# Kernel optimization log

Hardware: AMD Instinct MI355X
Metric: run time of the kernel (lower is better)

Reference implementation:

```python
import jax, jax.numpy as jnp
import numpy as np

INPUT_SIZE = 32
HIDDEN = 512
LAYERS = 2
B, T = 16, 2048


def _lstm_layer(x, w_ih, w_hh, b_ih, b_hh):
    """Single LSTM layer, batch_first. x: [B,T,I]. Gate order (PyTorch): i,f,g,o."""
    Bsz = x.shape[0]
    H = w_hh.shape[1]
    # Precompute input contribution for all timesteps: [B,T,4H]
    gx = jnp.einsum('bti,gi->btg', x, w_ih) + b_ih

    def step(carry, gx_t):
        h, c = carry
        g = gx_t + h @ w_hh.T + b_hh  # [B,4H]
        i, f, gg, o = jnp.split(g, 4, axis=-1)
        i = jax.nn.sigmoid(i)
        f = jax.nn.sigmoid(f)
        gg = jnp.tanh(gg)
        o = jax.nn.sigmoid(o)
        c = f * c + i * gg
        h = o * jnp.tanh(c)
        return (h, c), h

    h0 = jnp.zeros((Bsz, H), x.dtype)
    (hT, cT), hs = jax.lax.scan(step, (h0, h0), jnp.swapaxes(gx, 0, 1))
    return jnp.swapaxes(hs, 0, 1), hT, cT  # [B,T,H], [B,H], [B,H]


def setup_inputs() -> dict:
    key = jax.random.key(0)
    ks = jax.random.split(key, 11)
    s = 1.0 / np.sqrt(HIDDEN)  # PyTorch uniform init scale
    u = lambda k, shape: jax.random.uniform(k, shape, jnp.float32, -s, s)
    return {
        'x': jax.random.normal(ks[0], (B, T, INPUT_SIZE), jnp.float32),
        'w_ih0': u(ks[1], (4 * HIDDEN, INPUT_SIZE)),
        'w_hh0': u(ks[2], (4 * HIDDEN, HIDDEN)),
        'b_ih0': u(ks[3], (4 * HIDDEN,)),
        'b_hh0': u(ks[4], (4 * HIDDEN,)),
        'w_ih1': u(ks[5], (4 * HIDDEN, HIDDEN)),
        'w_hh1': u(ks[6], (4 * HIDDEN, HIDDEN)),
        'b_ih1': u(ks[7], (4 * HIDDEN,)),
        'b_hh1': u(ks[8], (4 * HIDDEN,)),
        'w_out': u(ks[9], (INPUT_SIZE, HIDDEN)),
        'b_out': u(ks[10], (INPUT_SIZE,)),
    }


def reference(x, w_ih0, w_hh0, b_ih0, b_hh0, w_ih1, w_hh1, b_ih1, b_hh1, w_out, b_out):
    h1, hT0, cT0 = _lstm_layer(x, w_ih0, w_hh0, b_ih0, b_hh0)
    h2, hT1, cT1 = _lstm_layer(h1, w_ih1, w_hh1, b_ih1, b_hh1)
    y = jnp.einsum('bth,oh->bto', h2, w_out) + b_out  # [B,T,input_size]
    h_n = jnp.stack([hT0, hT1], axis=0)  # [layers, B, H]
    c_n = jnp.stack([cT0, cT1], axis=0)
    return y, h_n, c_n
```

## Files before the change

kernel.cpp:

```cpp
#include <hip/hip_runtime.h>

#define TT   2048
#define NB   16
#define HH   512
#define NSL  32
#define HSL  16
#define KW   128
#define Y_SZ (NB*TT*32)
#define RING 256
#define RM   255

typedef __attribute__((ext_vector_type(8))) short bf16x8;
typedef __attribute__((ext_vector_type(4))) float f32x4;
typedef __attribute__((ext_vector_type(4))) unsigned u32x4;
typedef unsigned long long ull;

#define OFF_XCCV 0u
#define OFF_MODE 256u
#define OFF_PROG 512u
#define OFF_F1L  4096u
#define FLB      (4u*RING*32u*4u)
#define OFF_F1X  (OFF_F1L + FLB)
#define OFF_F2L  (OFF_F1X + FLB)
#define OFF_F2X  (OFF_F2L + FLB)
#define OFF_ZEND (OFF_F2X + FLB)
#define RSLOT    ((size_t)NB*HH)
#define RB       ((size_t)RING*RSLOT*2)
#define OFF_H1LH ((size_t)(1u<<20))
#define OFF_H1LL (OFF_H1LH + RB)
#define OFF_H1XH (OFF_H1LL + RB)
#define OFF_H1XL (OFF_H1XH + RB)
#define OFF_H2LH (OFF_H1XL + RB)
#define OFF_H2LL (OFF_H2LH + RB)
#define OFF_H2XH (OFF_H2LL + RB)
#define OFF_H2XL (OFF_H2XH + RB)
#define FB       ((size_t)TT*RSLOT*2)
#define OFF_H2FH (OFF_H2XL + RB)
#define OFF_H2FL (OFF_H2FH + FB)
#define WS_NEED  (OFF_H2FL + FB)

__device__ __forceinline__ unsigned short f2bf(float x){
  unsigned u = __float_as_uint(x);
  return (unsigned short)((u + 0x7FFFu + ((u >> 16) & 1u)) >> 16);
}
__device__ __forceinline__ float bf2f(unsigned short b){
  return __uint_as_float(((unsigned)b) << 16);
}
__device__ __forceinline__ float sigm(float v){ return 1.0f / (1.0f + __expf(-v)); }
__device__ __forceinline__ float tanh_f(float v){
  float a = fabsf(v);
  float e = __expf(-2.0f * a);
  float t = (1.0f - e) / (1.0f + e);
  return v < 0.0f ? -t : t;
}
__device__ __forceinline__ void split8(const float* __restrict__ p, bf16x8& hi, bf16x8& lo){
#pragma unroll
  for (int j = 0; j < 8; ++j){
    float w = p[j];
    unsigned short h = f2bf(w);
    hi[j] = (short)h;
    lo[j] = (short)f2bf(w - bf2f(h));
  }
}
__device__ __forceinline__ bf16x8 mk(ull a, ull b){
  union { ull u[2]; bf16x8 v; } r; r.u[0] = a; r.u[1] = b; return r.v;
}
__device__ __forceinline__ bf16x8 asfrag(u32x4 v){
  union { u32x4 u; bf16x8 b; } r; r.u = v; return r.b;
}
__device__ __forceinline__ ull ld64_lic(const ull* p){
  return __hip_atomic_load(p, __ATOMIC_RELAXED, __HIP_MEMORY_SCOPE_AGENT);
}
__device__ __forceinline__ unsigned ld32_lic(const unsigned* p){
  return __hip_atomic_load(p, __ATOMIC_RELAXED, __HIP_MEMORY_SCOPE_AGENT);
}
__device__ __forceinline__ void st64_lic(ull* p, ull v){
  __hip_atomic_store(p, v, __ATOMIC_RELAXED, __HIP_MEMORY_SCOPE_AGENT);
}
__device__ __forceinline__ void st32_lic(unsigned* p, unsigned v){
  __hip_atomic_store(p, v, __ATOMIC_RELAXED, __HIP_MEMORY_SCOPE_AGENT);
}
__device__ __forceinline__ bf16x8 ld_frag_lic(const unsigned short* p){
  return mk(ld64_lic((const ull*)p), ld64_lic((const ull*)p + 1));
}
__device__ __forceinline__ unsigned ld32_l2(const unsigned* p){
  unsigned r;
  asm volatile("buffer_inv sc0\n\t"
               "global_load_dword %0, %1, off\n\t"
               "s_waitcnt vmcnt(0)"
               : "=&v"(r) : "v"(p) : "memory");
  return r;
}
__device__ __forceinline__ void ld8_l2(const void* ph, const void* pl, u32x4* r){
  asm volatile(
    "buffer_inv sc0\n\t"
    "global_load_dwordx4 %0, %8, off\n\t"
    "global_load_dwordx4 %1, %8, off offset:64\n\t"
    "global_load_dwordx4 %2, %8, off offset:128\n\t"
    "global_load_dwordx4 %3, %8, off offset:192\n\t"
    "global_load_dwordx4 %4, %9, off\n\t"
    "global_load_dwordx4 %5, %9, off offset:64\n\t"
    "global_load_dwordx4 %6, %9, off offset:128\n\t"
    "global_load_dwordx4 %7, %9, off offset:192\n\t"
    "s_waitcnt vmcnt(0)"
    : "=&v"(r[0]),"=&v"(r[1]),"=&v"(r[2]),"=&v"(r[3]),
      "=&v"(r[4]),"=&v"(r[5]),"=&v"(r[6]),"=&v"(r[7])
    : "v"(ph), "v"(pl) : "memory");
}
__device__ __forceinline__ void ld8_lic(const void* ph, const void* pl, u32x4* r){
  asm volatile(
    "global_load_dwordx4 %0, %8, off sc0 sc1\n\t"
    "global_load_dwordx4 %1, %8, off offset:64 sc0 sc1\n\t"
    "global_load_dwordx4 %2, %8, off offset:128 sc0 sc1\n\t"
    "global_load_dwordx4 %3, %8, off offset:192 sc0 sc1\n\t"
    "global_load_dwordx4 %4, %9, off sc0 sc1\n\t"
    "global_load_dwordx4 %5, %9, off offset:64 sc0 sc1\n\t"
    "global_load_dwordx4 %6, %9, off offset:128 sc0 sc1\n\t"
    "global_load_dwordx4 %7, %9, off offset:192 sc0 sc1\n\t"
    "s_waitcnt vmcnt(0)"
    : "=&v"(r[0]),"=&v"(r[1]),"=&v"(r[2]),"=&v"(r[3]),
      "=&v"(r[4]),"=&v"(r[5]),"=&v"(r[6]),"=&v"(r[7])
    : "v"(ph), "v"(pl) : "memory");
}
__device__ __forceinline__ void st64_pl(void* p, ull v){
  asm volatile("global_store_dwordx2 %0, %1, off" :: "v"(p), "v"(v) : "memory");
}
__device__ __forceinline__ void st32_pl(unsigned* p, unsigned v){
  asm volatile("global_store_dword %0, %1, off" :: "v"(p), "v"(v) : "memory");
}

__device__ __forceinline__ int wait_hy(const unsigned* bL, const unsigned* bX,
                                       unsigned expect, int lane, int lmode, long& bud){
  if (!lmode){
    bool ok = (lane >= 32);
    while (__ballot(!ok) != 0ULL){
      if (!ok) ok = (ld32_lic(bX + lane) >= expect);
      if (--bud < 0) return 0;
    }
    return 0;
  }
  bool okL = (lane >= 32);
  int k = 0;
  while (true){
    if (__ballot(!okL) == 0ULL) return 1;
    if (!okL) okL = (ld32_l2(bL + lane) >= expect);
    if ((++k & 15) == 0){
      bool okX = (lane >= 32);
      if (!okX) okX = (ld32_lic(bX + lane) >= expect);
      if (__ballot(!okX) == 0ULL){
        if (!okL) okL = (ld32_l2(bL + lane) >= expect);
        return (__ballot(!okL) == 0ULL) ? 1 : 0;
      }
    }
    if (--bud < 0) return 0;
  }
}
__device__ __forceinline__ void wait_lic(const unsigned* bX, unsigned expect, int lane, long& bud){
  bool ok = (lane >= 32);
  while (__ballot(!ok) != 0ULL){
    if (!ok) ok = (ld32_lic(bX + lane) >= expect);
    if (--bud < 0) return;
  }
}

__global__ __launch_bounds__(256, 1) void lstm_persist(
    const float* __restrict__ x,
    const float* __restrict__ w_ih0, const float* __restrict__ w_hh0,
    const float* __restrict__ b_ih0, const float* __restrict__ b_hh0,
    const float* __restrict__ w_ih1, const float* __restrict__ w_hh1,
    const float* __restrict__ b_ih1, const float* __restrict__ b_hh1,
    float* __restrict__ out, unsigned char* __restrict__ ws)
{
  unsigned* XCCV = (unsigned*)(ws + OFF_XCCV);
  unsigned* MODE = (unsigned*)(ws + OFF_MODE);
  unsigned* PROG = (unsigned*)(ws + OFF_PROG);
  unsigned* F1L  = (unsigned*)(ws + OFF_F1L);
  unsigned* F1X  = (unsigned*)(ws + OFF_F1X);
  unsigned* F2L  = (unsigned*)(ws + OFF_F2L);
  unsigned* F2X  = (unsigned*)(ws + OFF_F2X);
  unsigned short* H1Lh = (unsigned short*)(ws + OFF_H1LH);
  unsigned short* H1Ll = (unsigned short*)(ws + OFF_H1LL);
  unsigned short* H1Xh = (unsigned short*)(ws + OFF_H1XH);
  unsigned short* H1Xl = (unsigned short*)(ws + OFF_H1XL);
  unsigned short* H2Lh = (unsigned short*)(ws + OFF_H2LH);
  unsigned short* H2Ll = (unsigned short*)(ws + OFF_H2LL);
  unsigned short* H2Xh = (unsigned short*)(ws + OFF_H2XH);
  unsigned short* H2Xl = (unsigned short*)(ws + OFF_H2XL);
  unsigned short* H2Fh = (unsigned short*)(ws + OFF_H2FH);
  unsigned short* H2Fl = (unsigned short*)(ws + OFF_H2FL);

  const int tid  = threadIdx.x;
  const int lane = tid & 63;
  const int wv   = tid >> 6;
  const int m16  = lane & 15;
  const int quad = lane >> 4;

  const int bid = blockIdx.x;
  const int xs  = bid & 7;
  const int pos = bid >> 3;
  if (xs >= 2 || pos >= NSL) return;
  const int layer = xs;
  const int sl    = pos;
  const int role  = layer * NSL + sl;
  const int j0    = sl * HSL;
  const int kwb   = wv * KW;

  long bud = 3000000;

  if (tid == 0){
    unsigned xcc = 0xDEAD;
    asm volatile("s_getreg_b32 %0, hwreg(HW_REG_XCC_ID)" : "=s"(xcc));
    st32_lic(XCCV + role, (xcc & 255u) | 0x100u);
  }
  __syncthreads();
  if (bid == 0 && wv == 0){
    bool got = false; unsigned v = 0;
    long b2 = 2000000;
    while (true){
      if (!got){ v = ld32_lic(XCCV + lane); got = (v & 0x100u) != 0u; }
      if (__ballot(!got) == 0ULL) break;
      if (--b2 < 0) break;
    }
    unsigned v0  = (unsigned)__shfl((int)v, 0, 64);
    unsigned v32 = (unsigned)__shfl((int)v, 32, 64);
    bool ok = got && ((lane < 32) ? (v == v0) : (v == v32));
    unsigned mode = (__ballot(!ok) == 0ULL) ? 1u : 0u;
    if (lane == 0) st32_lic(MODE, mode | 0x100u);
  }
  __shared__ unsigned s_mode;
  if (tid == 0){
    unsigned m = 0; long b3 = 2000000;
    do { m = ld32_lic(MODE); } while (!(m & 0x100u) && --b3 > 0);
    s_mode = m;
  }
  __syncthreads();
  int lmode = ((s_mode & 0x100u) && (s_mode & 1u)) ? 1 : 0;

  const float* Wh  = layer ? w_hh1 : w_hh0;
  const float* biL = layer ? b_ih1 : b_ih0;
  const float* bhL = layer ? b_hh1 : b_hh0;

  bf16x8 Bh_hi[4][4], Bh_lo[4][4];
#pragma unroll
  for (int g = 0; g < 4; ++g)
#pragma unroll
    for (int c = 0; c < 4; ++c){
      int row = g*HH + j0 + m16;
      int k0  = kwb + c*32 + quad*8;
      split8(Wh + (size_t)row*HH + k0, Bh_hi[g][c], Bh_lo[g][c]);
    }
  bf16x8 Bi_hi[4][4], Bi_lo[4][4];
  if (layer){
#pragma unroll
    for (int g = 0; g < 4; ++g)
#pragma unroll
      for (int c = 0; c < 4; ++c){
        int row = g*HH + j0 + m16;
        int k0  = kwb + c*32 + quad*8;
        split8(w_ih1 + (size_t)row*HH + k0, Bi_hi[g][c], Bi_lo[g][c]);
      }
  } else if (wv == 0){
#pragma unroll
    for (int g = 0; g < 4; ++g){
      int row = g*HH + j0 + m16;
      split8(w_ih0 + (size_t)row*32 + quad*8, Bi_hi[g][0], Bi_lo[g][0]);
    }
  }

  const int eb = tid >> 4;
  const int ej = tid & 15;
  float bias[4];
#pragma unroll
  for (int g = 0; g < 4; ++g){
    int r = g*HH + j0 + ej;
    bias[g] = biL[r] + bhL[r];
  }

  float cst = 0.0f;
  __shared__ float P[4][4][16][16];
  unsigned minp = 0;

  f32x4 accIn[4];
#pragma unroll
  for (int g = 0; g < 4; ++g) accIn[g] = f32x4{0.f, 0.f, 0.f, 0.f};
  if (layer){
    wait_lic(F1X + ((size_t)wv*RING + 1)*32, 1u, lane, bud);
    const size_t ib = ((size_t)1*NB + m16)*HH + kwb + quad*8;
    u32x4 r[8];
    ld8_lic(H1Xh + ib, H1Xl + ib, r);
#pragma unroll
    for (int c = 0; c < 4; ++c){
      bf16x8 ah = asfrag(r[c]);
      bf16x8 al = asfrag(r[4+c]);
#pragma unroll
      for (int g = 0; g < 4; ++g){
        accIn[g] = __builtin_amdgcn_mfma_f32_16x16x32_bf16(ah, Bi_hi[g][c], accIn[g], 0, 0, 0);
        accIn[g] = __builtin_amdgcn_mfma_f32_16x16x32_bf16(al, Bi_hi[g][c], accIn[g], 0, 0, 0);
        accIn[g] = __builtin_amdgcn_mfma_f32_16x16x32_bf16(ah, Bi_lo[g][c], accIn[g], 0, 0, 0);
      }
    }
  }

  for (int t = 0; t < TT; ++t){
    const unsigned srec = (unsigned)t & RM;
    const unsigned spub = (unsigned)(t+1) & RM;
    f32x4 acc[4];

    if (layer == 0){
#pragma unroll
      for (int g = 0; g < 4; ++g) acc[g] = f32x4{0.f, 0.f, 0.f, 0.f};
      if (wv == 0){
        const float* xp = x + ((size_t)m16*TT + t)*32 + quad*8;
        bf16x8 ah, al;
#pragma unroll
        for (int j = 0; j < 8; ++j){
          float v = xp[j];
          unsigned short h = f2bf(v);
          ah[j] = (short)h;
          al[j] = (short)f2bf(v - bf2f(h));
        }
#pragma unroll
        for (int g = 0; g < 4; ++g){
          acc[g] = __builtin_amdgcn_mfma_f32_16x16x32_bf16(ah, Bi_hi[g][0], acc[g], 0, 0, 0);
          acc[g] = __builtin_amdgcn_mfma_f32_16x16x32_bf16(al, Bi_hi[g][0], acc[g], 0, 0, 0);
          acc[g] = __builtin_amdgcn_mfma_f32_16x16x32_bf16(ah, Bi_lo[g][0], acc[g], 0, 0, 0);
        }
      }
      while ((long)(t+1) - (long)minp > 248L){
        unsigned v = (lane < 32) ? ld32_lic(PROG + lane) : 0xFFFFFFFFu;
        unsigned m = v;
#pragma unroll
        for (int o = 1; o < 32; o <<= 1){
          unsigned ov = (unsigned)__shfl_xor((int)m, o, 32);
          m = m < ov ? m : ov;
        }
        minp = (unsigned)__shfl((int)m, 0, 64);
        if (--bud < 0) break;
      }
      int got = lmode;
      if (t > 0){
        got = wait_hy(F1L + ((size_t)wv*RING + srec)*32,
                      F1X + ((size_t)wv*RING + srec)*32, (unsigned)t, lane, lmode, bud);
        if (!got) lmode = 0;
      }
      const size_t rb = ((size_t)srec*NB + m16)*HH + kwb + quad*8;
      u32x4 r[8];
      if (got) ld8_l2(H1Lh + rb, H1Ll + rb, r);
      else {
#pragma unroll
        for (int c = 0; c < 4; ++c){
          r[c]   = (u32x4)__builtin_bit_cast(u32x4, ld_frag_lic(H1Xh + rb + c*32));
          r[4+c] = (u32x4)__builtin_bit_cast(u32x4, ld_frag_lic(H1Xl + rb + c*32));
        }
      }
#pragma unroll
      for (int c = 0; c < 4; ++c){
        bf16x8 ah = asfrag(r[c]);
        bf16x8 al = asfrag(r[4+c]);
#pragma unroll
        for (int g = 0; g < 4; ++g){
          acc[g] = __builtin_amdgcn_mfma_f32_16x16x32_bf16(ah, Bh_hi[g][c], acc[g], 0, 0, 0);
          acc[g] = __builtin_amdgcn_mfma_f32_16x16x32_bf16(al, Bh_hi[g][c], acc[g], 0, 0, 0);
          acc[g] = __builtin_amdgcn_mfma_f32_16x16x32_bf16(ah, Bh_lo[g][c], acc[g], 0, 0, 0);
        }
      }
    } else {
#pragma unroll
      for (int g = 0; g < 4; ++g) acc[g] = accIn[g];
      int got = lmode;
      if (t > 0){
        got = wait_hy(F2L + ((size_t)wv*RING + srec)*32,
                      F2X + ((size_t)wv*RING + srec)*32, (unsigned)t, lane, lmode, bud);
        if (!got) lmode = 0;
      }
      const size_t rb = ((size_t)srec*NB + m16)*HH + kwb + quad*8;
      u32x4 r[8];
      if (got) ld8_l2(H2Lh + rb, H2Ll + rb, r);
      else {
#pragma unroll
        for (int c = 0; c < 4; ++c){
          r[c]   = (u32x4)__builtin_bit_cast(u32x4, ld_frag_lic(H2Xh + rb + c*32));
          r[4+c] = (u32x4)__builtin_bit_cast(u32x4, ld_frag_lic(H2Xl + rb + c*32));
        }
      }
#pragma unroll
      for (int c = 0; c < 4; ++c){
        bf16x8 ah = asfrag(r[c]);
        bf16x8 al = asfrag(r[4+c]);
#pragma unroll
        for (int g = 0; g < 4; ++g){
          acc[g] = __builtin_amdgcn_mfma_f32_16x16x32_bf16(ah, Bh_hi[g][c], acc[g], 0, 0, 0);
          acc[g] = __builtin_amdgcn_mfma_f32_16x16x32_bf16(al, Bh_hi[g][c], acc[g], 0, 0, 0);
          acc[g] = __builtin_amdgcn_mfma_f32_16x16x32_bf16(ah, Bh_lo[g][c], acc[g], 0, 0, 0);
        }
      }
    }

#pragma unroll
    for (int g = 0; g < 4; ++g)
#pragma unroll
      for (int r = 0; r < 4; ++r)
        P[wv][g][quad*4 + r][m16] = acc[g][r];
    __syncthreads();

    float G[4];
#pragma unroll
    for (int g = 0; g < 4; ++g)
      G[g] = P[0][g][eb][ej] + P[1][g][eb][ej] + P[2][g][eb][ej] + P[3][g][eb][ej] + bias[g];

    float gi = sigm(G[0]);
    float gf = sigm(G[1]);
    float gc = tanh_f(G[2]);
    float go = sigm(G[3]);
    cst = gf*cst + gi*gc;
    float h = go * tanh_f(cst);

    if (t == TT-1){
      size_t o = (size_t)layer*NB*HH + (size_t)eb*HH + (j0 + ej);
      out[Y_SZ + o] = h;
      out[Y_SZ + 2*NB*HH + o] = cst;
    }

    unsigned short hhi = f2bf(h);
    unsigned short hlo = f2bf(h - bf2f(hhi));
    ull h1s = (ull)(unsigned short)__shfl_down((int)hhi, 1, 64);
    ull h2s = (ull)(unsigned short)__shfl_down((int)hhi, 2, 64);
    ull h3s = (ull)(unsigned short)__shfl_down((int)hhi, 3, 64);
    ull l1s = (ull)(unsigned short)__shfl_down((int)hlo, 1, 64);
    ull l2s = (ull)(unsigned short)__shfl_down((int)hlo, 2, 64);
    ull l3s = (ull)(unsigned short)__shfl_down((int)hlo, 3, 64);
    if ((ej & 3) == 0){
      ull vh = (ull)hhi | (h1s << 16) | (h2s << 32) | (h3s << 48);
      ull vl = (ull)hlo | (l1s << 16) | (l2s << 32) | (l3s << 48);
      size_t pr = (((size_t)spub*NB + eb)*HH + (unsigned)(j0 + ej)) >> 2;
      if (layer == 0){
        st64_pl((ull*)H1Lh + pr, vh);
        st64_pl((ull*)H1Ll + pr, vl);
        st64_lic((ull*)H1Xh + pr, vh);
        st64_lic((ull*)H1Xl + pr, vl);
      } else {
        size_t pf_ = (((size_t)t*NB + eb)*HH + (unsigned)(j0 + ej)) >> 2;
        st64_pl((ull*)H2Lh + pr, vh);
        st64_pl((ull*)H2Ll + pr, vl);
        st64_pl((ull*)H2Fh + pf_, vh);
        st64_pl((ull*)H2Fl + pf_, vl);
        st64_lic((ull*)H2Xh + pr, vh);
        st64_lic((ull*)H2Xl + pr, vl);
      }
    }

    asm volatile("s_waitcnt vmcnt(2)" ::: "memory");
    __syncthreads();
    if (tid == 0){
      unsigned val = (unsigned)(t+1);
      unsigned* FL = layer ? F2L : F1L;
#pragma unroll
      for (int r2 = 0; r2 < 4; ++r2)
        st32_pl(FL + ((size_t)r2*RING + spub)*32 + sl, val);
    }
    asm volatile("s_waitcnt vmcnt(0)" ::: "memory");
    __syncthreads();
    if (tid == 0){
      unsigned val = (unsigned)(t+1);
      unsigned* FX = layer ? F2X : F1X;
#pragma unroll
      for (int r2 = 0; r2 < 4; ++r2)
        st32_lic(FX + ((size_t)r2*RING + spub)*32 + sl, val);
      if (layer) st32_lic(PROG + sl, val);
    }

    if (layer && t + 1 < TT){
#pragma unroll
      for (int g = 0; g < 4; ++g) accIn[g] = f32x4{0.f, 0.f, 0.f, 0.f};
      const unsigned nslot = (unsigned)(t+2) & RM;
      wait_lic(F1X + ((size_t)wv*RING + nslot)*32, (unsigned)(t+2), lane, bud);
      const size_t nb_ = ((size_t)nslot*NB + m16)*HH + kwb + quad*8;
      u32x4 r[8];
      ld8_lic(H1Xh + nb_, H1Xl + nb_, r);
#pragma unroll
      for (int c = 0; c < 4; ++c){
        bf16x8 ah = asfrag(r[c]);
        bf16x8 al = asfrag(r[4+c]);
#pragma unroll
        for (int g = 0; g < 4; ++g){
          accIn[g] = __builtin_amdgcn_mfma_f32_16x16x32_bf16(ah, Bi_hi[g][c], accIn[g], 0, 0, 0);
          accIn[g] = __builtin_amdgcn_mfma_f32_16x16x32_bf16(al, Bi_hi[g][c], accIn[g], 0, 0, 0);
          accIn[g] = __builtin_amdgcn_mfma_f32_16x16x32_bf16(ah, Bi_lo[g][c], accIn[g], 0, 0, 0);
        }
      }
    }
  }
}

__global__ __launch_bounds__(256, 1) void y_proj(
    const unsigned short* __restrict__ Hhi2, const unsigned short* __restrict__ Hlo2,
    const float* __restrict__ w_out, const float* __restrict__ b_out,
    float* __restrict__ out)
{
  __shared__ float hsh[NB][HH + 1];
  __shared__ float wsh[32][HH + 1];
  const int tid = threadIdx.x;
  const int t = blockIdx.x;

  for (int i = tid; i < 32*HH; i += 256){
    int o = i >> 9, k = i & (HH-1);
    wsh[o][k] = w_out[i];
  }
  for (int i = tid; i < NB*HH; i += 256){
    int b = i >> 9, k = i & (HH-1);
    size_t off = ((size_t)t*NB + b)*HH + k;
    hsh[b][k] = bf2f(Hhi2[off]) + bf2f(Hlo2[off]);
  }
  __syncthreads();

  const int o = tid & 31, bg = tid >> 5;
  float a0 = 0.f, a1 = 0.f;
  for (int k = 0; k < HH; ++k){
    float w = wsh[o][k];
    a0 += w * hsh[bg][k];
    a1 += w * hsh[bg + 8][k];
  }
  float bo = b_out[o];
  out[((size_t)bg*TT + t)*32 + o] = a0 + bo;
  out[((size_t)(bg+8)*TT + t)*32 + o] = a1 + bo;
}

extern "C" void kernel_launch(void* const* d_in, const int* in_sizes, int n_in,
                              void* d_out, int out_size, void* d_ws, size_t ws_size,
                              hipStream_t stream)
{
  (void)in_sizes; (void)n_in; (void)out_size;
  const float* x     = (const float*)d_in[0];
  const float* w_ih0 = (const float*)d_in[1];
  const float* w_hh0 = (const float*)d_in[2];
  const float* b_ih0 = (const float*)d_in[3];
  const float* b_hh0 = (const float*)d_in[4];
  const float* w_ih1 = (const float*)d_in[5];
  const float* w_hh1 = (const float*)d_in[6];
  const float* b_ih1 = (const float*)d_in[7];
  const float* b_hh1 = (const float*)d_in[8];
  const float* w_out = (const float*)d_in[9];
  const float* b_out = (const float*)d_in[10];
  float* out = (float*)d_out;
  unsigned char* ws = (unsigned char*)d_ws;

  if (ws_size < WS_NEED) return;

  hipMemsetAsync(ws, 0, OFF_ZEND, stream);
  hipMemsetAsync(ws + OFF_H1LH, 0, RSLOT*2, stream);
  hipMemsetAsync(ws + OFF_H1LL, 0, RSLOT*2, stream);
  hipMemsetAsync(ws + OFF_H1XH, 0, RSLOT*2, stream);
  hipMemsetAsync(ws + OFF_H1XL, 0, RSLOT*2, stream);
  hipMemsetAsync(ws + OFF_H2LH, 0, RSLOT*2, stream);
  hipMemsetAsync(ws + OFF_H2LL, 0, RSLOT*2, stream);
  hipMemsetAsync(ws + OFF_H2XH, 0, RSLOT*2, stream);
  hipMemsetAsync(ws + OFF_H2XL, 0, RSLOT*2, stream);

  lstm_persist<<<dim3(512), dim3(256), 0, stream>>>(
      x, w_ih0, w_hh0, b_ih0, b_hh0, w_ih1, w_hh1, b_ih1, b_hh1, out, ws);

  const unsigned short* H2Fh = (const unsigned short*)(ws + OFF_H2FH);
  const unsigned short* H2Fl = (const unsigned short*)(ws + OFF_H2FL);
  y_proj<<<dim3(TT), dim3(256), 0, stream>>>(H2Fh, H2Fl, w_out, b_out, out);
}
```

Measured before the change: 10.08 ms.

## Overlap layer-1 input prefetch with flag publish and batch cross-layer waits

For layer 1, the step now issues the next timestep's layer-0 hidden-state loads before the cross-block flag barrier, so they overlap with the F2X publish. It also waits for layer-0 progress up to 16 steps ahead, so the per-step flag polling happens only occasionally. The LDS scratch array is padded to 17 columns to avoid bank conflicts, and __syncthreads is replaced by raw s_barrier with explicit waitcnt. This adds ordering subtlety: the relaxed waitcnt counts and the raw barriers must still keep the memory visibility that the protocol needs.

```diff
diff --git a/kernel.cpp b/kernel.cpp
--- a/kernel.cpp
+++ b/kernel.cpp
@@ -118,6 +118,20 @@
     "global_load_dwordx4 %6, %9, off offset:128 sc0 sc1\n\t"
     "global_load_dwordx4 %7, %9, off offset:192 sc0 sc1\n\t"
     "s_waitcnt vmcnt(0)"
+    : "=&v"(r[0]),"=&v"(r[1]),"=&v"(r[2]),"=&v"(r[3]),
+      "=&v"(r[4]),"=&v"(r[5]),"=&v"(r[6]),"=&v"(r[7])
+    : "v"(ph), "v"(pl) : "memory");
+}
+__device__ __forceinline__ void ld8_lic_issue(const void* ph, const void* pl, u32x4* r){
+  asm volatile(
+    "global_load_dwordx4 %0, %8, off sc0 sc1\n\t"
+    "global_load_dwordx4 %1, %8, off offset:64 sc0 sc1\n\t"
+    "global_load_dwordx4 %2, %8, off offset:128 sc0 sc1\n\t"
+    "global_load_dwordx4 %3, %8, off offset:192 sc0 sc1\n\t"
+    "global_load_dwordx4 %4, %9, off sc0 sc1\n\t"
+    "global_load_dwordx4 %5, %9, off offset:64 sc0 sc1\n\t"
+    "global_load_dwordx4 %6, %9, off offset:128 sc0 sc1\n\t"
+    "global_load_dwordx4 %7, %9, off offset:192 sc0 sc1"
     : "=&v"(r[0]),"=&v"(r[1]),"=&v"(r[2]),"=&v"(r[3]),
       "=&v"(r[4]),"=&v"(r[5]),"=&v"(r[6]),"=&v"(r[7])
     : "v"(ph), "v"(pl) : "memory");
@@ -277,14 +291,16 @@
   }
 
   float cst = 0.0f;
-  __shared__ float P[4][4][16][16];
+  __shared__ float P[4][4][16][17];
   unsigned minp = 0;
+  unsigned f1seen = 0;
 
   f32x4 accIn[4];
 #pragma unroll
   for (int g = 0; g < 4; ++g) accIn[g] = f32x4{0.f, 0.f, 0.f, 0.f};
   if (layer){
     wait_lic(F1X + ((size_t)wv*RING + 1)*32, 1u, lane, bud);
+    f1seen = 1u;
     const size_t ib = ((size_t)1*NB + m16)*HH + kwb + quad*8;
     u32x4 r[8];
     ld8_lic(H1Xh + ib, H1Xl + ib, r);
@@ -449,43 +465,65 @@
       }
     }
 
-    asm volatile("s_waitcnt vmcnt(2)" ::: "memory");
-    __syncthreads();
-    if (tid == 0){
-      unsigned val = (unsigned)(t+1);
-      unsigned* FL = layer ? F2L : F1L;
-#pragma unroll
-      for (int r2 = 0; r2 < 4; ++r2)
-        st32_pl(FL + ((size_t)r2*RING + spub)*32 + sl, val);
-    }
-    asm volatile("s_waitcnt vmcnt(0)" ::: "memory");
-    __syncthreads();
-    if (tid == 0){
-      unsigned val = (unsigned)(t+1);
-      unsigned* FX = layer ? F2X : F1X;
-#pragma unroll
-      for (int r2 = 0; r2 < 4; ++r2)
-        st32_lic(FX + ((size_t)r2*RING + spub)*32 + sl, val);
-      if (layer) st32_lic(PROG + sl, val);
-    }
-
-    if (layer && t + 1 < TT){
-#pragma unroll
-      for (int g = 0; g < 4; ++g) accIn[g] = f32x4{0.f, 0.f, 0.f, 0.f};
-      const unsigned nslot = (unsigned)(t+2) & RM;
-      wait_lic(F1X + ((size_t)wv*RING + nslot)*32, (unsigned)(t+2), lane, bud);
-      const size_t nb_ = ((size_t)nslot*NB + m16)*HH + kwb + quad*8;
-      u32x4 r[8];
-      ld8_lic(H1Xh + nb_, H1Xl + nb_, r);
-#pragma unroll
-      for (int c = 0; c < 4; ++c){
-        bf16x8 ah = asfrag(r[c]);
-        bf16x8 al = asfrag(r[4+c]);
-#pragma unroll
-        for (int g = 0; g < 4; ++g){
-          accIn[g] = __builtin_amdgcn_mfma_f32_16x16x32_bf16(ah, Bi_hi[g][c], accIn[g], 0, 0, 0);
-          accIn[g] = __builtin_amdgcn_mfma_f32_16x16x32_bf16(al, Bi_hi[g][c], accIn[g], 0, 0, 0);
-          accIn[g] = __builtin_amdgcn_mfma_f32_16x16x32_bf16(ah, Bi_lo[g][c], accIn[g], 0, 0, 0);
+    if (layer == 0){
+      asm volatile("s_waitcnt vmcnt(2) lgkmcnt(0)" ::: "memory");
+      __builtin_amdgcn_s_barrier();
+      if (tid == 0){
+        unsigned val = (unsigned)(t+1);
+#pragma unroll
+        for (int r2 = 0; r2 < 4; ++r2)
+          st32_pl(F1L + ((size_t)r2*RING + spub)*32 + sl, val);
+      }
+      asm volatile("s_waitcnt vmcnt(0)" ::: "memory");
+      __builtin_amdgcn_s_barrier();
+      if (tid == 0){
+        unsigned val = (unsigned)(t+1);
+#pragma unroll
+        for (int r2 = 0; r2 < 4; ++r2)
+          st32_lic(F1X + ((size_t)r2*RING + spub)*32 + sl, val);
+      }
+    } else {
+      asm volatile("s_waitcnt vmcnt(4) lgkmcnt(0)" ::: "memory");
+      __builtin_amdgcn_s_barrier();
+      if (tid == 0){
+        unsigned val = (unsigned)(t+1);
+#pragma unroll
+        for (int r2 = 0; r2 < 4; ++r2)
+          st32_pl(F2L + ((size_t)r2*RING + spub)*32 + sl, val);
+      }
+      if (t + 1 < TT){
+        if (f1seen < (unsigned)(t+2)){
+          unsigned tgt = (unsigned)(t + 17);
+          if (tgt > (unsigned)TT) tgt = (unsigned)TT;
+          wait_lic(F1X + ((size_t)wv*RING + (tgt & RM))*32, tgt, lane, bud);
+          f1seen = tgt;
+        }
+        const unsigned nslot = (unsigned)(t+2) & RM;
+        const size_t nb_ = ((size_t)nslot*NB + m16)*HH + kwb + quad*8;
+        u32x4 rr[8];
+        ld8_lic_issue(H1Xh + nb_, H1Xl + nb_, rr);
+        asm volatile("s_waitcnt vmcnt(0)" ::: "memory");
+        __builtin_amdgcn_sched_barrier(0);
+        __builtin_amdgcn_s_barrier();
+        if (tid == 0){
+          unsigned val = (unsigned)(t+1);
+#pragma unroll
+          for (int r2 = 0; r2 < 4; ++r2)
+            st32_lic(F2X + ((size_t)r2*RING + spub)*32 + sl, val);
+          st32_lic(PROG + sl, val);
+        }
+#pragma unroll
+        for (int g = 0; g < 4; ++g) accIn[g] = f32x4{0.f, 0.f, 0.f, 0.f};
+#pragma unroll
+        for (int c = 0; c < 4; ++c){
+          bf16x8 ah = asfrag(rr[c]);
+          bf16x8 al = asfrag(rr[4+c]);
+#pragma unroll
+          for (int g = 0; g < 4; ++g){
+            accIn[g] = __builtin_amdgcn_mfma_f32_16x16x32_bf16(ah, Bi_hi[g][c], accIn[g], 0, 0, 0);
+            accIn[g] = __builtin_amdgcn_mfma_f32_16x16x32_bf16(al, Bi_hi[g][c], accIn[g], 0, 0, 0);
+            accIn[g] = __builtin_amdgcn_mfma_f32_16x16x32_bf16(ah, Bi_lo[g][c], accIn[g], 0, 0, 0);
+          }
         }
       }
     }
```

Result: no change. 10.06 ms (-0.3%).
